# Kernel tuning notes

Measured on AMD Instinct MI355X. Metric: run time of the kernel, lower is better.

The kernel has to match this reference:

```python
import jax, jax.numpy as jnp
import numpy as np

EMBED_DIM = 32  # module-level constant used for the 1/sqrt(d) scale in the source
DROP_P = 0.2


def setup_inputs() -> dict:
    key = jax.random.key(0)
    kx, kq, kk, kv = jax.random.split(key, 4)
    B, T, C = 8, 4096, EMBED_DIM
    x = jax.random.normal(kx, (B, T, C), dtype=jnp.float32)
    Wq = jax.random.normal(kq, (C, C), dtype=jnp.float32) * (1.0 / np.sqrt(C))
    Wk = jax.random.normal(kk, (C, C), dtype=jnp.float32) * (1.0 / np.sqrt(C))
    Wv = jax.random.normal(kv, (C, C), dtype=jnp.float32) * (1.0 / np.sqrt(C))
    return {"x": x, "Wq": Wq, "Wk": Wk, "Wv": Wv}


def reference(x, Wq, Wk, Wv):
    B, T, C = x.shape
    # bias-free linear projections: y = x @ W.T (torch nn.Linear convention)
    q = jnp.einsum('btc,dc->btd', x, Wq)
    k = jnp.einsum('btc,dc->btd', x, Wk)
    v = jnp.einsum('btc,dc->btd', x, Wv)
    # scaled scores [B, T, T]
    att = jnp.einsum('btd,bsd->bts', q, k) / jnp.sqrt(jnp.float32(EMBED_DIM))
    causal = jnp.tril(jnp.ones((T, T), dtype=bool))
    att = jnp.where(causal, att, -jnp.inf)
    wei = jax.nn.softmax(att, axis=-1)
    # dropout on attention weights (training mode, p=0.2), deterministic key
    keep = jax.random.bernoulli(jax.random.key(42), 1.0 - DROP_P, wei.shape)
    wei = jnp.where(keep, wei / (1.0 - DROP_P), 0.0)
    return jnp.einsum('bts,bsd->btd', wei, v)
```

## Files before the change

kernel.cpp:

```cpp
#include <hip/hip_runtime.h>
#include <stdint.h>

#define BB 8
#define TTN 4096
#define CCH 32
#define WIN 128
#define KEEP_LT9 3435974144u

typedef __attribute__((ext_vector_type(8))) short bf16x8;
typedef __attribute__((ext_vector_type(4))) float f32x4;

union B8 { uint32_t u[4]; uint4 q; bf16x8 v; };

__device__ __forceinline__ uint32_t cvt_pk_bf16(float lo, float hi) {
    uint32_t d;
    asm("v_cvt_pk_bf16_f32 %0, %1, %2" : "=v"(d) : "v"(lo), "v"(hi));
    return d;
}

__device__ __forceinline__ uint32_t rotl32(uint32_t x, int r) {
    return __builtin_amdgcn_alignbit(x, x, 32 - r);
}

__device__ __forceinline__ void threefry2x32_k042(uint32_t x0, uint32_t x1,
                                                  uint32_t& o0, uint32_t& o1) {
    const uint32_t k0 = 0u, k1 = 42u;
    const uint32_t k2 = 0u ^ 42u ^ 0x1BD11BDAu;
    x0 += k0; x1 += k1;
#define TFR(r) { x0 += x1; x1 = rotl32(x1, (r)); x1 ^= x0; }
    TFR(13) TFR(15) TFR(26) TFR(6)
    x0 += k1; x1 += k2 + 1u;
    TFR(17) TFR(29) TFR(16) TFR(24)
    x0 += k2; x1 += k0 + 2u;
    TFR(13) TFR(15) TFR(26) TFR(6)
    x0 += k0; x1 += k1 + 3u;
    TFR(17) TFR(29) TFR(16) TFR(24)
    x0 += k1; x1 += k2 + 4u;
    TFR(13) TFR(15) TFR(26) TFR(6)
    x0 += k2; x1 += k0 + 5u;
#undef TFR
    o0 = x0; o1 = x1;
}

__device__ __forceinline__ uint32_t mask_bits(uint32_t idx) {
    uint32_t o0, o1; threefry2x32_k042(0u, idx, o0, o1); return o0 ^ o1;
}

__global__ __launch_bounds__(256) void proj_qkv(const float* __restrict__ x,
                                                const float* __restrict__ Wq,
                                                const float* __restrict__ Wk,
                                                const float* __restrict__ Wv,
                                                float* __restrict__ Qf,
                                                uint16_t* __restrict__ Kb,
                                                uint16_t* __restrict__ Vt) {
    __shared__ float sW[3][CCH * CCH];
    __shared__ uint16_t vs[256][34];
    const int tid = threadIdx.x;
    for (int i = tid; i < CCH * CCH; i += 256) {
        sW[0][i] = Wq[i]; sW[1][i] = Wk[i]; sW[2][i] = Wv[i];
    }
    __syncthreads();
    const int row = blockIdx.x * 256 + tid;
    const float4* xp = reinterpret_cast<const float4*>(x + (size_t)row * CCH);
    float xr[CCH];
    #pragma unroll
    for (int i = 0; i < 8; ++i) {
        float4 t4 = xp[i];
        xr[4*i] = t4.x; xr[4*i+1] = t4.y; xr[4*i+2] = t4.z; xr[4*i+3] = t4.w;
    }
    const float scale = 0.17677669529663687f;
    #pragma unroll
    for (int mtx = 0; mtx < 3; ++mtx) {
        float o[CCH];
        #pragma unroll
        for (int d = 0; d < CCH; ++d) {
            float s0 = 0.f, s1 = 0.f, s2 = 0.f, s3 = 0.f;
            #pragma unroll
            for (int c = 0; c < CCH; c += 4) {
                s0 += xr[c]   * sW[mtx][d*CCH + c];
                s1 += xr[c+1] * sW[mtx][d*CCH + c+1];
                s2 += xr[c+2] * sW[mtx][d*CCH + c+2];
                s3 += xr[c+3] * sW[mtx][d*CCH + c+3];
            }
            o[d] = (s0 + s1) + (s2 + s3);
            if (mtx == 0) o[d] *= scale;
        }
        if (mtx == 0) {
            float4* op = reinterpret_cast<float4*>(Qf + (size_t)row * CCH);
            #pragma unroll
            for (int i = 0; i < 8; ++i)
                op[i] = make_float4(o[4*i], o[4*i+1], o[4*i+2], o[4*i+3]);
        } else if (mtx == 1) {
            uint32_t dw[16];
            #pragma unroll
            for (int k = 0; k < 16; ++k) dw[k] = cvt_pk_bf16(o[2*k], o[2*k+1]);
            uint4* kp = reinterpret_cast<uint4*>((char*)Kb + (size_t)row * 64);
            #pragma unroll
            for (int q = 0; q < 4; ++q)
                kp[q] = make_uint4(dw[4*q], dw[4*q+1], dw[4*q+2], dw[4*q+3]);
        } else {
            #pragma unroll
            for (int k = 0; k < 16; ++k)
                *reinterpret_cast<uint32_t*>(&vs[tid][2*k]) = cvt_pk_bf16(o[2*k], o[2*k+1]);
        }
    }
    __syncthreads();
    const int b = blockIdx.x >> 4, seg = blockIdx.x & 15;
    const int d = tid >> 3, part = tid & 7;
    uint32_t dw[16];
    #pragma unroll
    for (int k = 0; k < 16; ++k) {
        const uint32_t lo = vs[part*32 + 2*k][d];
        const uint32_t hi = vs[part*32 + 2*k + 1][d];
        dw[k] = lo | (hi << 16);
    }
    uint16_t* dst = Vt + (size_t)b * (CCH * TTN) + (size_t)d * TTN + seg * 256 + part * 32;
    uint4* dp = reinterpret_cast<uint4*>(dst);
    #pragma unroll
    for (int q = 0; q < 4; ++q)
        dp[q] = make_uint4(dw[4*q], dw[4*q+1], dw[4*q+2], dw[4*q+3]);
}

__global__ __launch_bounds__(512, 4) void attn_mfma(const float* __restrict__ Qf,
                                                    const uint16_t* __restrict__ Kb,
                                                    const uint16_t* __restrict__ Vt,
                                                    float* __restrict__ out) {
    __shared__ __align__(16) char smem[33792];

    const int j = blockIdx.x;
    const int b = j & 7;
    const int tile = 127 - (j >> 3);
    const int w = threadIdx.x >> 6;
    const int lane = threadIdx.x & 63;
    const int tl = lane & 15;
    const int g = lane >> 4;
    const int thalf = w & 1;
    const int sg = w >> 1;
    const int slb = sg * 32;
    const int t0 = tile * 32;
    const int t_g = t0 + thalf * 16 + tl;

    const float* qrow = Qf + ((size_t)b * TTN + t_g) * CCH + g * 8;
    const float4 qa = *reinterpret_cast<const float4*>(qrow);
    const float4 qb = *reinterpret_cast<const float4*>(qrow + 4);
    B8 qf;
    qf.u[0] = cvt_pk_bf16(qa.x, qa.y); qf.u[1] = cvt_pk_bf16(qa.z, qa.w);
    qf.u[2] = cvt_pk_bf16(qb.x, qb.y); qf.u[3] = cvt_pk_bf16(qb.z, qb.w);

    f32x4 acc0 = {0.f,0.f,0.f,0.f}, acc1 = {0.f,0.f,0.f,0.f};
    float m = -1e30f, l = 0.f;

    const char* Kbb = (const char*)Kb + (size_t)b * TTN * 64;
    const char* Vbb = (const char*)Vt + (size_t)b * CCH * TTN * 2;
    const uint32_t idxb = ((uint32_t)b << 24) | ((uint32_t)t_g << 12);

    const int nwin = (32 * tile + 159) >> 7;

    uint4 sgK, sgV;
    const int krow_st = threadIdx.x >> 2, koff_st = (threadIdx.x & 3) * 16;
    const int vrow_st = threadIdx.x >> 4, voff_st = (threadIdx.x & 15) * 16;

#define ISSUE_KV(S0)                                                           \
    {                                                                          \
        sgK = *reinterpret_cast<const uint4*>(Kbb + (size_t)((S0) + krow_st) * 64 + koff_st); \
        sgV = *reinterpret_cast<const uint4*>(Vbb + (size_t)vrow_st * 8192 + (size_t)(S0) * 2 + voff_st); \
    }
#define WRITE_KV(D)                                                            \
    {                                                                          \
        char* base = smem + (D) * 16896;                                       \
        *reinterpret_cast<uint4*>(base + krow_st * 64 + koff_st) = sgK;        \
        *reinterpret_cast<uint4*>(base + 8192 + vrow_st * 272 + voff_st) = sgV; \
    }

#define ATT_WINDOW(D, S0, TAIL)                                                \
    {                                                                          \
        const char* kb = smem + (D) * 16896;                                   \
        const char* vb = kb + 8192;                                            \
        B8 ka, kc, va, vc, pf;                                                 \
        ka.q = *reinterpret_cast<const uint4*>(kb + (slb + tl) * 64 + g * 16); \
        kc.q = *reinterpret_cast<const uint4*>(kb + (slb + 16 + tl) * 64 + g * 16); \
        va.q = *reinterpret_cast<const uint4*>(vb + tl * 272 + (slb + g * 8) * 2); \
        vc.q = *reinterpret_cast<const uint4*>(vb + (16 + tl) * 272 + (slb + g * 8) * 2); \
        const f32x4 zz = {0.f,0.f,0.f,0.f};                                    \
        f32x4 d0 = __builtin_amdgcn_mfma_f32_16x16x32_bf16(ka.v, qf.v, zz, 0, 0, 0); \
        f32x4 d1 = __builtin_amdgcn_mfma_f32_16x16x32_bf16(kc.v, qf.v, zz, 0, 0, 0); \
        if (TAIL) {                                                            \
            const int sv = (S0) + slb + 4 * g;                                 \
            d0.x = (sv + 0  <= t_g) ? d0.x : -1e30f;                           \
            d0.y = (sv + 1  <= t_g) ? d0.y : -1e30f;                           \
            d0.z = (sv + 2  <= t_g) ? d0.z : -1e30f;                           \
            d0.w = (sv + 3  <= t_g) ? d0.w : -1e30f;                           \
            d1.x = (sv + 16 <= t_g) ? d1.x : -1e30f;                           \
            d1.y = (sv + 17 <= t_g) ? d1.y : -1e30f;                           \
            d1.z = (sv + 18 <= t_g) ? d1.z : -1e30f;                           \
            d1.w = (sv + 19 <= t_g) ? d1.w : -1e30f;                           \
        }                                                                      \
        float mx = fmaxf(fmaxf(fmaxf(d0.x, d0.y), fmaxf(d0.z, d0.w)),          \
                         fmaxf(fmaxf(d1.x, d1.y), fmaxf(d1.z, d1.w)));         \
        mx = fmaxf(mx, __shfl_xor(mx, 16));                                    \
        mx = fmaxf(mx, __shfl_xor(mx, 32));                                    \
        const bool up = mx > m + 8.0f;               \
        const float corr = up ? __expf(m - mx) : 1.0f;                         \
        m = up ? mx : m;                                                       \
        l *= corr; acc0 *= corr; acc1 *= corr;                                 \
        float p0 = __expf(d0.x - m), p1 = __expf(d0.y - m);                    \
        float p2 = __expf(d0.z - m), p3 = __expf(d0.w - m);                    \
        float p4 = __expf(d1.x - m), p5 = __expf(d1.y - m);                    \
        float p6 = __expf(d1.z - m), p7 = __expf(d1.w - m);                    \
        if (TAIL) {                                                            \
            const float alive = ((S0) + slb <= t_g) ? 1.0f : 0.0f;             \
            p0 *= alive; p1 *= alive; p2 *= alive; p3 *= alive;                \
            p4 *= alive; p5 *= alive; p6 *= alive; p7 *= alive;                \
        }                                                                      \
        float ls = ((p0 + p1) + (p2 + p3)) + ((p4 + p5) + (p6 + p7));          \
        ls += __shfl_xor(ls, 16);                                              \
        ls += __shfl_xor(ls, 32);                                              \
        l += ls;                                                               \
              \
        const uint32_t ib = idxb | (uint32_t)((S0) + slb + 4 * g);             \
        const float q0 = (mask_bits(ib + 0)  < KEEP_LT9) ? p0 : 0.f;           \
        const float q1 = (mask_bits(ib + 1)  < KEEP_LT9) ? p1 : 0.f;           \
        const float q2 = (mask_bits(ib + 2)  < KEEP_LT9) ? p2 : 0.f;           \
        const float q3 = (mask_bits(ib + 3)  < KEEP_LT9) ? p3 : 0.f;           \
        const float q4 = (mask_bits(ib + 16) < KEEP_LT9) ? p4 : 0.f;           \
        const float q5 = (mask_bits(ib + 17) < KEEP_LT9) ? p5 : 0.f;           \
        const float q6 = (mask_bits(ib + 18) < KEEP_LT9) ? p6 : 0.f;           \
        const float q7 = (mask_bits(ib + 19) < KEEP_LT9) ? p7 : 0.f;           \
        const uint32_t k00 = cvt_pk_bf16(q0, q1), k01 = cvt_pk_bf16(q2, q3);   \
        const uint32_t k10 = cvt_pk_bf16(q4, q5), k11 = cvt_pk_bf16(q6, q7);   \
        const int srcA = 16 * ((g & 1) * 2) + tl;                              \
        const int srcB = srcA + 16;                                            \
        const uint32_t a0 = (uint32_t)__shfl((int)k00, srcA);                  \
        const uint32_t b0 = (uint32_t)__shfl((int)k10, srcA);                  \
        const uint32_t a1 = (uint32_t)__shfl((int)k01, srcA);                  \
        const uint32_t b1 = (uint32_t)__shfl((int)k11, srcA);                  \
        const uint32_t a2 = (uint32_t)__shfl((int)k00, srcB);                  \
        const uint32_t b2 = (uint32_t)__shfl((int)k10, srcB);                  \
        const uint32_t a3 = (uint32_t)__shfl((int)k01, srcB);                  \
        const uint32_t b3 = (uint32_t)__shfl((int)k11, srcB);                  \
        const bool hi = (g >= 2);                                              \
        pf.u[0] = hi ? b0 : a0; pf.u[1] = hi ? b1 : a1;                        \
        pf.u[2] = hi ? b2 : a2; pf.u[3] = hi ? b3 : a3;                        \
        acc0 = __builtin_amdgcn_mfma_f32_16x16x32_bf16(va.v, pf.v, acc0, 0, 0, 0); \
        acc1 = __builtin_amdgcn_mfma_f32_16x16x32_bf16(vc.v, pf.v, acc1, 0, 0, 0); \
    }

    ISSUE_KV(0)
    WRITE_KV(0)
    __syncthreads();

    int buf = 0;
    for (int win = 0; win < nwin - 1; ++win) {
        const int s0 = win << 7;
        ISSUE_KV(s0 + WIN)
        ATT_WINDOW(buf, s0, 0)
        WRITE_KV(buf ^ 1)
        __syncthreads();
        buf ^= 1;
    }
    {
        const int s0 = (nwin - 1) << 7;
        if (s0 + slb <= t0 + thalf * 16 + 15) ATT_WINDOW(buf, s0, 1)
        __syncthreads();
    }
#undef ATT_WINDOW
#undef ISSUE_KV
#undef WRITE_KV

#define SLOT(TH, S) reinterpret_cast<float*>(smem + ((TH) * 2 + (S)) * 2432)
#define PUBLISH(SB)                                                            \
    {                                                                          \
        float* sb = (SB);                                                      \
        *reinterpret_cast<float4*>(sb + tl * 36 + 4 * g)      = make_float4(acc0.x, acc0.y, acc0.z, acc0.w); \
        *reinterpret_cast<float4*>(sb + tl * 36 + 16 + 4 * g) = make_float4(acc1.x, acc1.y, acc1.z, acc1.w); \
        if (g == 0) { sb[576 + 2 * tl] = m; sb[577 + 2 * tl] = l; }            \
    }
#define CONSUME(SB)                                                            \
    {                                                                          \
        const float* sb = (SB);                                                \
        const float m2 = sb[576 + 2 * tl], l2 = sb[577 + 2 * tl];              \
        const float4 x0 = *reinterpret_cast<const float4*>(sb + tl * 36 + 4 * g); \
        const float4 x1 = *reinterpret_cast<const float4*>(sb + tl * 36 + 16 + 4 * g); \
        const float mn = fmaxf(m, m2);                                         \
        const float ca = __expf(m - mn), cb = __expf(m2 - mn);                 \
        l = l * ca + l2 * cb;                                                  \
        acc0.x = acc0.x * ca + x0.x * cb; acc0.y = acc0.y * ca + x0.y * cb;    \
        acc0.z = acc0.z * ca + x0.z * cb; acc0.w = acc0.w * ca + x0.w * cb;    \
        acc1.x = acc1.x * ca + x1.x * cb; acc1.y = acc1.y * ca + x1.y * cb;    \
        acc1.z = acc1.z * ca + x1.z * cb; acc1.w = acc1.w * ca + x1.w * cb;    \
        m = mn;                                                                \
    }
    if (sg >= 2) PUBLISH(SLOT(thalf, sg - 2))
    __syncthreads();
    if (sg < 2) CONSUME(SLOT(thalf, sg))
    __syncthreads();
    if (sg == 1) PUBLISH(SLOT(thalf, 0))
    __syncthreads();
    if (sg == 0) {
        CONSUME(SLOT(thalf, 0))
        const float inv = 1.0f / (0.8f * l);
        float* orow = out + ((size_t)b * TTN + t_g) * CCH;
        *reinterpret_cast<float4*>(orow + 4 * g) =
            make_float4(acc0.x * inv, acc0.y * inv, acc0.z * inv, acc0.w * inv);
        *reinterpret_cast<float4*>(orow + 16 + 4 * g) =
            make_float4(acc1.x * inv, acc1.y * inv, acc1.z * inv, acc1.w * inv);
    }
#undef SLOT
#undef PUBLISH
#undef CONSUME
}

extern "C" void kernel_launch(void* const* d_in, const int* in_sizes, int n_in,
                              void* d_out, int out_size, void* d_ws, size_t ws_size,
                              hipStream_t stream) {
    const float* x  = (const float*)d_in[0];
    const float* Wq = (const float*)d_in[1];
    const float* Wk = (const float*)d_in[2];
    const float* Wv = (const float*)d_in[3];
    float* outp = (float*)d_out;

    float*    Qf = (float*)d_ws;
    uint16_t* Kb = (uint16_t*)((char*)d_ws + 4194304);
    uint16_t* Vt = (uint16_t*)((char*)d_ws + 6291456);

    proj_qkv<<<(BB * TTN) / 256, 256, 0, stream>>>(x, Wq, Wk, Wv, Qf, Kb, Vt);
    attn_mfma<<<1024, 512, 0, stream>>>(Qf, Kb, Vt, outp);
}
```

Before: 175.3 us.

## Load K/V directly from global, interleave threefry, rebalance causal tile order

Removes the shared-memory double-buffered K/V staging and its per-window barriers, so each wave loads its K and V fragments straight from global memory (relying on cache) and LDS shrinks to what the final merge needs. The dropout threefry hash is now computed four lanes at a time and hoisted before the score MFMAs, which gives more instruction-level parallelism and lets the hash overlap the matrix ops. The block-to-tile mapping is changed to interleave long and short causal tiles for better load balance. The risks are redundant global/L2 traffic across waves and higher register pressure.

```diff
diff --git a/kernel.cpp b/kernel.cpp
--- a/kernel.cpp
+++ b/kernel.cpp
@@ -22,28 +22,50 @@
     return __builtin_amdgcn_alignbit(x, x, 32 - r);
 }
 
-__device__ __forceinline__ void threefry2x32_k042(uint32_t x0, uint32_t x1,
-                                                  uint32_t& o0, uint32_t& o1) {
-    const uint32_t k0 = 0u, k1 = 42u;
-    const uint32_t k2 = 0u ^ 42u ^ 0x1BD11BDAu;
-    x0 += k0; x1 += k1;
+__device__ __forceinline__ uint32_t mask_bits(uint32_t idx) {
+    uint32_t x0 = 0u, x1 = idx + 42u;
+    const uint32_t K2 = 42u ^ 0x1BD11BDAu;
 #define TFR(r) { x0 += x1; x1 = rotl32(x1, (r)); x1 ^= x0; }
     TFR(13) TFR(15) TFR(26) TFR(6)
-    x0 += k1; x1 += k2 + 1u;
+    x0 += 42u; x1 += K2 + 1u;
     TFR(17) TFR(29) TFR(16) TFR(24)
-    x0 += k2; x1 += k0 + 2u;
+    x0 += K2; x1 += 2u;
     TFR(13) TFR(15) TFR(26) TFR(6)
-    x0 += k0; x1 += k1 + 3u;
+    x1 += 42u + 3u;
     TFR(17) TFR(29) TFR(16) TFR(24)
-    x0 += k1; x1 += k2 + 4u;
+    x0 += 42u; x1 += K2 + 4u;
     TFR(13) TFR(15) TFR(26) TFR(6)
-    x0 += k2; x1 += k0 + 5u;
+    x0 += K2; x1 += 5u;
 #undef TFR
-    o0 = x0; o1 = x1;
-}
-
-__device__ __forceinline__ uint32_t mask_bits(uint32_t idx) {
-    uint32_t o0, o1; threefry2x32_k042(0u, idx, o0, o1); return o0 ^ o1;
+    return x0 ^ x1;
+}
+
+__device__ __forceinline__ void threefry4(uint32_t i0, uint32_t i1, uint32_t i2, uint32_t i3,
+                                          uint32_t& o0, uint32_t& o1, uint32_t& o2, uint32_t& o3) {
+    const uint32_t K2 = 42u ^ 0x1BD11BDAu;
+    uint32_t a0 = 0u, a1 = 0u, a2 = 0u, a3 = 0u;
+    uint32_t b0 = i0 + 42u, b1 = i1 + 42u, b2 = i2 + 42u, b3 = i3 + 42u;
+#define R4(r)                                                                  \
+    { a0 += b0; a1 += b1; a2 += b2; a3 += b3;                                  \
+      b0 = rotl32(b0, (r)); b1 = rotl32(b1, (r));                              \
+      b2 = rotl32(b2, (r)); b3 = rotl32(b3, (r));                              \
+      b0 ^= a0; b1 ^= a1; b2 ^= a2; b3 ^= a3; }
+#define INJ(da, db)                                                            \
+    { a0 += (da); a1 += (da); a2 += (da); a3 += (da);                          \
+      b0 += (db); b1 += (db); b2 += (db); b3 += (db); }
+    R4(13) R4(15) R4(26) R4(6)
+    INJ(42u, K2 + 1u)
+    R4(17) R4(29) R4(16) R4(24)
+    INJ(K2, 2u)
+    R4(13) R4(15) R4(26) R4(6)
+    INJ(0u, 42u + 3u)
+    R4(17) R4(29) R4(16) R4(24)
+    INJ(42u, K2 + 4u)
+    R4(13) R4(15) R4(26) R4(6)
+    INJ(K2, 5u)
+#undef R4
+#undef INJ
+    o0 = a0 ^ b0; o1 = a1 ^ b1; o2 = a2 ^ b2; o3 = a3 ^ b3;
 }
 
 __global__ __launch_bounds__(256) void proj_qkv(const float* __restrict__ x,
@@ -125,11 +147,14 @@
                                                     const uint16_t* __restrict__ Kb,
                                                     const uint16_t* __restrict__ Vt,
                                                     float* __restrict__ out) {
-    __shared__ __align__(16) char smem[33792];
+    __shared__ __align__(16) char smem[9728];
 
     const int j = blockIdx.x;
     const int b = j & 7;
-    const int tile = 127 - (j >> 3);
+    const int u = j >> 3;
+    const int tile = (u < 32) ? (127 - u) : (u < 64) ? (u - 32)
+                   : (u < 96) ? (159 - u) : (u - 64);
+
     const int w = threadIdx.x >> 6;
     const int lane = threadIdx.x & 63;
     const int tl = lane & 15;
@@ -156,36 +181,32 @@
 
     const int nwin = (32 * tile + 159) >> 7;
 
-    uint4 sgK, sgV;
-    const int krow_st = threadIdx.x >> 2, koff_st = (threadIdx.x & 3) * 16;
-    const int vrow_st = threadIdx.x >> 4, voff_st = (threadIdx.x & 15) * 16;
-
-#define ISSUE_KV(S0)                                                           \
+#define ATT_WINDOW(S0, TAIL)                                                   \
     {                                                                          \
-        sgK = *reinterpret_cast<const uint4*>(Kbb + (size_t)((S0) + krow_st) * 64 + koff_st); \
-        sgV = *reinterpret_cast<const uint4*>(Vbb + (size_t)vrow_st * 8192 + (size_t)(S0) * 2 + voff_st); \
-    }
-#define WRITE_KV(D)                                                            \
-    {                                                                          \
-        char* base = smem + (D) * 16896;                                       \
-        *reinterpret_cast<uint4*>(base + krow_st * 64 + koff_st) = sgK;        \
-        *reinterpret_cast<uint4*>(base + 8192 + vrow_st * 272 + voff_st) = sgV; \
-    }
-
-#define ATT_WINDOW(D, S0, TAIL)                                                \
-    {                                                                          \
-        const char* kb = smem + (D) * 16896;                                   \
-        const char* vb = kb + 8192;                                            \
+        const int srow = (S0) + slb;                                           \
         B8 ka, kc, va, vc, pf;                                                 \
-        ka.q = *reinterpret_cast<const uint4*>(kb + (slb + tl) * 64 + g * 16); \
-        kc.q = *reinterpret_cast<const uint4*>(kb + (slb + 16 + tl) * 64 + g * 16); \
-        va.q = *reinterpret_cast<const uint4*>(vb + tl * 272 + (slb + g * 8) * 2); \
-        vc.q = *reinterpret_cast<const uint4*>(vb + (16 + tl) * 272 + (slb + g * 8) * 2); \
+        ka.q = *reinterpret_cast<const uint4*>(Kbb + (size_t)(srow + tl) * 64 + g * 16); \
+        kc.q = *reinterpret_cast<const uint4*>(Kbb + (size_t)(srow + 16 + tl) * 64 + g * 16); \
+        va.q = *reinterpret_cast<const uint4*>(Vbb + (size_t)tl * 8192 + (size_t)(srow + g * 8) * 2); \
+        vc.q = *reinterpret_cast<const uint4*>(Vbb + (size_t)(16 + tl) * 8192 + (size_t)(srow + g * 8) * 2); \
+              \
+        const uint32_t ib = idxb | (uint32_t)(srow + 4 * g);                   \
+        uint32_t r0, r1, r2, r3, r4, r5, r6, r7;                               \
+        threefry4(ib,       ib + 1u,  ib + 2u,  ib + 3u,  r0, r1, r2, r3);     \
+        threefry4(ib + 16u, ib + 17u, ib + 18u, ib + 19u, r4, r5, r6, r7);     \
+        const float f0 = (r0 < KEEP_LT9) ? 1.f : 0.f;                          \
+        const float f1 = (r1 < KEEP_LT9) ? 1.f : 0.f;                          \
+        const float f2 = (r2 < KEEP_LT9) ? 1.f : 0.f;                          \
+        const float f3 = (r3 < KEEP_LT9) ? 1.f : 0.f;                          \
+        const float f4 = (r4 < KEEP_LT9) ? 1.f : 0.f;                          \
+        const float f5 = (r5 < KEEP_LT9) ? 1.f : 0.f;                          \
+        const float f6 = (r6 < KEEP_LT9) ? 1.f : 0.f;                          \
+        const float f7 = (r7 < KEEP_LT9) ? 1.f : 0.f;                          \
         const f32x4 zz = {0.f,0.f,0.f,0.f};                                    \
         f32x4 d0 = __builtin_amdgcn_mfma_f32_16x16x32_bf16(ka.v, qf.v, zz, 0, 0, 0); \
         f32x4 d1 = __builtin_amdgcn_mfma_f32_16x16x32_bf16(kc.v, qf.v, zz, 0, 0, 0); \
         if (TAIL) {                                                            \
-            const int sv = (S0) + slb + 4 * g;                                 \
+            const int sv = srow + 4 * g;                                       \
             d0.x = (sv + 0  <= t_g) ? d0.x : -1e30f;                           \
             d0.y = (sv + 1  <= t_g) ? d0.y : -1e30f;                           \
             d0.z = (sv + 2  <= t_g) ? d0.z : -1e30f;                           \
@@ -208,7 +229,7 @@
         float p4 = __expf(d1.x - m), p5 = __expf(d1.y - m);                    \
         float p6 = __expf(d1.z - m), p7 = __expf(d1.w - m);                    \
         if (TAIL) {                                                            \
-            const float alive = ((S0) + slb <= t_g) ? 1.0f : 0.0f;             \
+            const float alive = (srow <= t_g) ? 1.0f : 0.0f;                   \
             p0 *= alive; p1 *= alive; p2 *= alive; p3 *= alive;                \
             p4 *= alive; p5 *= alive; p6 *= alive; p7 *= alive;                \
         }                                                                      \
@@ -216,18 +237,10 @@
         ls += __shfl_xor(ls, 16);                                              \
         ls += __shfl_xor(ls, 32);                                              \
         l += ls;                                                               \
-              \
-        const uint32_t ib = idxb | (uint32_t)((S0) + slb + 4 * g);             \
-        const float q0 = (mask_bits(ib + 0)  < KEEP_LT9) ? p0 : 0.f;           \
-        const float q1 = (mask_bits(ib + 1)  < KEEP_LT9) ? p1 : 0.f;           \
-        const float q2 = (mask_bits(ib + 2)  < KEEP_LT9) ? p2 : 0.f;           \
-        const float q3 = (mask_bits(ib + 3)  < KEEP_LT9) ? p3 : 0.f;           \
-        const float q4 = (mask_bits(ib + 16) < KEEP_LT9) ? p4 : 0.f;           \
-        const float q5 = (mask_bits(ib + 17) < KEEP_LT9) ? p5 : 0.f;           \
-        const float q6 = (mask_bits(ib + 18) < KEEP_LT9) ? p6 : 0.f;           \
-        const float q7 = (mask_bits(ib + 19) < KEEP_LT9) ? p7 : 0.f;           \
-        const uint32_t k00 = cvt_pk_bf16(q0, q1), k01 = cvt_pk_bf16(q2, q3);   \
-        const uint32_t k10 = cvt_pk_bf16(q4, q5), k11 = cvt_pk_bf16(q6, q7);   \
+        const uint32_t k00 = cvt_pk_bf16(p0 * f0, p1 * f1);                    \
+        const uint32_t k01 = cvt_pk_bf16(p2 * f2, p3 * f3);                    \
+        const uint32_t k10 = cvt_pk_bf16(p4 * f4, p5 * f5);                    \
+        const uint32_t k11 = cvt_pk_bf16(p6 * f6, p7 * f7);                    \
         const int srcA = 16 * ((g & 1) * 2) + tl;                              \
         const int srcB = srcA + 16;                                            \
         const uint32_t a0 = (uint32_t)__shfl((int)k00, srcA);                  \
@@ -245,27 +258,15 @@
         acc1 = __builtin_amdgcn_mfma_f32_16x16x32_bf16(vc.v, pf.v, acc1, 0, 0, 0); \
     }
 
-    ISSUE_KV(0)
-    WRITE_KV(0)
-    __syncthreads();
-
-    int buf = 0;
+    #pragma unroll 1
     for (int win = 0; win < nwin - 1; ++win) {
-        const int s0 = win << 7;
-        ISSUE_KV(s0 + WIN)
-        ATT_WINDOW(buf, s0, 0)
-        WRITE_KV(buf ^ 1)
-        __syncthreads();
-        buf ^= 1;
+        ATT_WINDOW(win << 7, 0)
     }
     {
         const int s0 = (nwin - 1) << 7;
-        if (s0 + slb <= t0 + thalf * 16 + 15) ATT_WINDOW(buf, s0, 1)
-        __syncthreads();
+        if (s0 + slb <= t0 + thalf * 16 + 15) ATT_WINDOW(s0, 1)
     }
 #undef ATT_WINDOW
-#undef ISSUE_KV
-#undef WRITE_KV
 
 #define SLOT(TH, S) reinterpret_cast<float*>(smem + ((TH) * 2 + (S)) * 2432)
 #define PUBLISH(SB)                                                            \
```

After: 168.2 us. -4.0%, faster.
